# Performance work log

Measured on AMD Instinct MI355X. Metric: run time of the kernel, lower is better.

The kernel has to match this reference:

```python
import jax, jax.numpy as jnp
import numpy as np

B, T, F, H = 256, 128, 32, 1024  # batch, seq_len(=decoder steps), input/output feat, hidden


def lstm_cell(x, h, c, Wih, Whh, b):
    # PyTorch gate order: i, f, g, o
    gates = x @ Wih.T + h @ Whh.T + b  # [B, 4H]
    i, f, g, o = jnp.split(gates, 4, axis=-1)
    i, f, o = jax.nn.sigmoid(i), jax.nn.sigmoid(f), jax.nn.sigmoid(o)
    c_new = f * c + i * jnp.tanh(g)
    h_new = o * jnp.tanh(c_new)
    return h_new, c_new


def setup_inputs() -> dict:
    key = jax.random.key(0)
    ks = jax.random.split(key, 16)
    s = 0.05
    d = {
        "input_seq": jax.random.normal(ks[0], (B, T, F), jnp.float32),
        # encoder LSTM (2 layers); bias = bias_ih + bias_hh folded together
        "enc_Wih0": jax.random.normal(ks[1], (4 * H, F), jnp.float32) * s,
        "enc_Whh0": jax.random.normal(ks[2], (4 * H, H), jnp.float32) * s,
        "enc_b0": jax.random.normal(ks[3], (4 * H,), jnp.float32) * s,
        "enc_Wih1": jax.random.normal(ks[4], (4 * H, H), jnp.float32) * s,
        "enc_Whh1": jax.random.normal(ks[5], (4 * H, H), jnp.float32) * s,
        "enc_b1": jax.random.normal(ks[6], (4 * H,), jnp.float32) * s,
        # decoder LSTM (2 layers), input size = output_size = F
        "dec_Wih0": jax.random.normal(ks[7], (4 * H, F), jnp.float32) * s,
        "dec_Whh0": jax.random.normal(ks[8], (4 * H, H), jnp.float32) * s,
        "dec_b0": jax.random.normal(ks[9], (4 * H,), jnp.float32) * s,
        "dec_Wih1": jax.random.normal(ks[10], (4 * H, H), jnp.float32) * s,
        "dec_Whh1": jax.random.normal(ks[11], (4 * H, H), jnp.float32) * s,
        "dec_b1": jax.random.normal(ks[12], (4 * H,), jnp.float32) * s,
        # output head
        "lin_W": jax.random.normal(ks[13], (F, H), jnp.float32) * s,
        "lin_b": jax.random.normal(ks[14], (F,), jnp.float32) * s,
    }
    return d


def reference(input_seq, enc_Wih0, enc_Whh0, enc_b0, enc_Wih1, enc_Whh1, enc_b1,
              dec_Wih0, dec_Whh0, dec_b0, dec_Wih1, dec_Whh1, dec_b1, lin_W, lin_b):
    Bsz = input_seq.shape[0]
    zeros = jnp.zeros((Bsz, H), input_seq.dtype)

    # ---- encoder: 2-layer LSTM scanned over time ----
    def enc_step(carry, x_t):
        h0, c0, h1, c1 = carry
        h0, c0 = lstm_cell(x_t, h0, c0, enc_Wih0, enc_Whh0, enc_b0)
        h1, c1 = lstm_cell(h0, h1, c1, enc_Wih1, enc_Whh1, enc_b1)
        return (h0, c0, h1, c1), None

    xs = jnp.swapaxes(input_seq, 0, 1)  # [T, B, F]
    (h0, c0, h1, c1), _ = jax.lax.scan(enc_step, (zeros, zeros, zeros, zeros), xs)

    def dec_step(carry, _):
        x, h0, c0, h1, c1 = carry
        h0, c0 = lstm_cell(x, h0, c0, dec_Wih0, dec_Whh0, dec_b0)
        h1, c1 = lstm_cell(h0, h1, c1, dec_Wih1, dec_Whh1, dec_b1)
        out = h1 @ lin_W.T + lin_b  # [B, F]
        return (out, h0, c0, h1, c1), out

    dec_in0 = input_seq[:, -1, :]  # [B, F]
    _, outs = jax.lax.scan(dec_step, (dec_in0, h0, c0, h1, c1), None, length=T)
    return jnp.swapaxes(outs, 0, 1)  # [B, T, F]
```

## Files before the change

kernel.cpp:

```cpp
#include <hip/hip_runtime.h>

typedef _Float16 half_t;
typedef _Float16 half8 __attribute__((ext_vector_type(8)));
typedef _Float16 half4v __attribute__((ext_vector_type(4)));
typedef float f32x4 __attribute__((ext_vector_type(4)));

#define DI __device__ __forceinline__

constexpr int Bsz = 256;
constexpr int Tsz = 128;
constexpr int Fsz = 32;
constexpr int Hsz = 1024;
constexpr int NG  = 4096;
constexpr int K1  = 1152;
constexpr int K2  = 2048;

DI int perm_to_orig(int np) {
    int nt = np >> 6, r = np & 63, g = r >> 4, jo = r & 15;
    return g * Hsz + nt * 16 + jo;
}

DI size_t wfrag(int np, int k) {
    return ((size_t)((k >> 5) * 256 + (np >> 4)) * 64 + ((k >> 3) & 3) * 16 + (np & 15)) * 8 + (k & 7);
}
DI size_t afrag(int b, int k) {
    return ((size_t)((k >> 5) * 16 + (b >> 4)) * 64 + ((k >> 3) & 3) * 16 + (b & 15)) * 8 + (k & 7);
}


__global__ void pack_cat(half_t* __restrict__ dst, const float* __restrict__ srcA, int KA,
                         const float* __restrict__ srcB, int KB, int KP) {
    int tid = threadIdx.x;
    int np = blockIdx.y * 64 + (tid & 63);
    int k0 = (blockIdx.x * 4 + (tid >> 6)) * 8;
    if (k0 >= KP) return;
    int n = perm_to_orig(np);
    half8 v;
#pragma unroll
    for (int j = 0; j < 8; ++j) {
        int k = k0 + j;
        float f = 0.f;
        if (k < KA) f = srcA[(size_t)n * KA + k];
        else if (k < KA + KB) f = srcB[(size_t)n * KB + (k - KA)];
        v[j] = (half_t)f;
    }
    *(half8*)(dst + wfrag(np, k0)) = v;
}

__global__ void pack_fold(half_t* __restrict__ dst, const float* __restrict__ Wih0,
                          const float* __restrict__ linW) {
    __shared__ float lw[32][128];
    __shared__ float wi[16][32];
    int nb = blockIdx.x * 16;
    int jb = blockIdx.y * 128;
    int t = threadIdx.x;
    for (int i = t; i < 32 * 128; i += 256) { int f = i >> 7, j = i & 127; lw[f][j] = linW[f * Hsz + jb + j]; }
    for (int i = t; i < 16 * 32; i += 256) { int r = i >> 5, f = i & 31; wi[r][f] = Wih0[perm_to_orig(nb + r) * 32 + f]; }
    __syncthreads();
    int r = t >> 4, j0 = (t & 15) * 8;
    half8 v;
#pragma unroll
    for (int jj = 0; jj < 8; ++jj) {
        float s = 0.f;
#pragma unroll
        for (int f = 0; f < 32; ++f) s += wi[r][f] * lw[f][j0 + jj];
        v[jj] = (half_t)s;
    }
    *(half8*)(dst + wfrag(nb + r, 1024 + jb + j0)) = v;
}

__global__ void pack_bias(float* __restrict__ b5, const float* eb0, const float* eb1,
                          const float* db0, const float* db1, const float* dWih0,
                          const float* linb) {
    int idx = blockIdx.x * 256 + threadIdx.x;
    if (idx >= 5 * NG) return;
    int which = idx >> 12, np = idx & (NG - 1);
    int n = perm_to_orig(np);
    float v;
    if (which == 0) v = eb0[n];
    else if (which == 1) v = eb1[n];
    else if (which == 2) v = db0[n];
    else if (which == 3) {
        v = db0[n];
        for (int f = 0; f < 32; ++f) v += dWih0[n * 32 + f] * linb[f];
    } else v = db1[n];
    b5[idx] = v;
}

__global__ void pack_small(half_t* __restrict__ Wlin, half_t* __restrict__ bufA0,
                           const float* __restrict__ linW, const float* __restrict__ inseq) {
    int idx = blockIdx.x * 256 + threadIdx.x;
    if (idx < 32 * Hsz) Wlin[idx] = (half_t)linW[idx];
    if (idx < Bsz * 4) {
        int b = idx >> 2, fg = idx & 3;
        half8 v;
#pragma unroll
        for (int j = 0; j < 8; ++j) v[j] = (half_t)inseq[(size_t)b * (Tsz * Fsz) + fg * 8 + j];
        *(half8*)(bufA0 + afrag(b, 1024 + fg * 8)) = v;
    }
}


template <int K>
__launch_bounds__(256, 1) __global__
void lstm_phase(const half_t* __restrict__ A, const half_t* __restrict__ W,
                const float* __restrict__ bias, float* __restrict__ c,
                half_t* __restrict__ hd0, int cb0,
                half_t* __restrict__ hd1, int cb1,
                half_t* __restrict__ hd2, int cb2,
                const float* __restrict__ xsrc, half_t* __restrict__ xdst) {
    constexpr int CHW = (K / 32) / 4;
    __shared__ float red[4][64][68];
    int bid = blockIdx.x;
    int low3 = bid & 7, rest = bid >> 3;
    int mt = rest & 3, nt = ((rest >> 2) << 3) | low3;
    int tid = threadIdx.x, lane = tid & 63, w = tid >> 6;

    const half_t* pa = A + ((size_t)((w * CHW) * 16 + mt * 4) * 64 + lane) * 8;
    const half_t* pw = W + ((size_t)((w * CHW) * 256 + nt * 4) * 64 + lane) * 8;

    f32x4 acc[4][4] = {};
    half8 bA[3][4], bW[3][4];

#define LOADS(st, kk)                                                              \
    {                                                                              \
        _Pragma("unroll") for (int mi = 0; mi < 4; ++mi)                           \
            bA[st][mi] = *(const half8*)(pa + (size_t)(kk) * 8192 + mi * 512);     \
        _Pragma("unroll") for (int ni = 0; ni < 4; ++ni)                           \
            bW[st][ni] = *(const half8*)(pw + (size_t)(kk) * 131072 + ni * 512);   \
    }

    LOADS(0, 0)
    LOADS(1, 1)
#pragma unroll
    for (int kk = 0; kk < CHW; ++kk) {
        if (kk + 2 < CHW) LOADS((kk + 2) % 3, kk + 2)
        const int st = kk % 3;
#pragma unroll
        for (int mi = 0; mi < 4; ++mi)
#pragma unroll
            for (int ni = 0; ni < 4; ++ni)
                acc[mi][ni] = __builtin_amdgcn_mfma_f32_16x16x32_f16(bA[st][mi], bW[st][ni], acc[mi][ni], 0, 0, 0);
    }
#undef LOADS

    int l15 = lane & 15, l4 = lane >> 4;
#pragma unroll
    for (int mi = 0; mi < 4; ++mi)
#pragma unroll
        for (int ni = 0; ni < 4; ++ni)
#pragma unroll
            for (int r = 0; r < 4; ++r)
                red[w][mi * 16 + l4 * 4 + r][ni * 16 + l15] = acc[mi][ni][r];
    __syncthreads();

    int row = tid >> 2, q = tid & 3, jo0 = q * 4;
    f32x4 g0 = {}, g1 = {}, g2 = {}, g3 = {};
#pragma unroll
    for (int ww = 0; ww < 4; ++ww) {
        g0 += *(const f32x4*)&red[ww][row][jo0];
        g1 += *(const f32x4*)&red[ww][row][16 + jo0];
        g2 += *(const f32x4*)&red[ww][row][32 + jo0];
        g3 += *(const f32x4*)&red[ww][row][48 + jo0];
    }
    const float* bb = bias + nt * 64;
    g0 += *(const f32x4*)(bb + jo0);
    g1 += *(const f32x4*)(bb + 16 + jo0);
    g2 += *(const f32x4*)(bb + 32 + jo0);
    g3 += *(const f32x4*)(bb + 48 + jo0);

    int bglob = mt * 64 + row;
    int jg0 = nt * 16 + jo0;
    float* cp = c + (size_t)bglob * Hsz + jg0;
    f32x4 cold = *(const f32x4*)cp;
    f32x4 cnew;
    half4v hv;
#pragma unroll
    for (int e = 0; e < 4; ++e) {
        float si = 1.f / (1.f + __expf(-g0[e]));
        float sf = 1.f / (1.f + __expf(-g1[e]));
        float tg = 1.f - 2.f / (__expf(2.f * g2[e]) + 1.f);
        float so = 1.f / (1.f + __expf(-g3[e]));
        float cn = sf * cold[e] + si * tg;
        cnew[e] = cn;
        float th = 1.f - 2.f / (__expf(2.f * cn) + 1.f);
        hv[e] = (half_t)(so * th);
    }
    *(f32x4*)cp = cnew;

    {
        int col = cb0 + jg0;
        *(half4v*)(hd0 + ((size_t)((col >> 5) * 16 + (bglob >> 4)) * 64 + ((col >> 3) & 3) * 16 + (bglob & 15)) * 8 + (col & 7)) = hv;
    }
    if (hd1) {
        int col = cb1 + jg0;
        *(half4v*)(hd1 + ((size_t)((col >> 5) * 16 + (bglob >> 4)) * 64 + ((col >> 3) & 3) * 16 + (bglob & 15)) * 8 + (col & 7)) = hv;
    }
    if (hd2) {
        int col = cb2 + jg0;
        *(half4v*)(hd2 + ((size_t)((col >> 5) * 16 + (bglob >> 4)) * 64 + ((col >> 3) & 3) * 16 + (bglob & 15)) * 8 + (col & 7)) = hv;
    }

    if (xsrc && nt == 0) {
        int f0 = q * 8;
        const float* xs = xsrc + (size_t)bglob * (Tsz * Fsz) + f0;
        half8 v;
#pragma unroll
        for (int j = 0; j < 8; ++j) v[j] = (half_t)xs[j];
        *(half8*)(xdst + afrag(bglob, 1024 + f0)) = v;
    }
}

__launch_bounds__(256, 1) __global__
void lin_out(const half_t* __restrict__ H1, const half_t* __restrict__ Wl,
             const float* __restrict__ lb, float* __restrict__ out) {
    int w = threadIdx.x >> 6, lane = threadIdx.x & 63;
    int l15 = lane & 15, l4 = lane >> 4;
    int rowt = blockIdx.x * 4 + w;
    int t = rowt >> 4, mi = rowt & 15;
    const half_t* pa = H1 + (size_t)t * (Bsz * Hsz);
    const half_t* pb0 = Wl + (size_t)l15 * Hsz + l4 * 8;
    const half_t* pb1 = Wl + (size_t)(16 + l15) * Hsz + l4 * 8;
    f32x4 ac0 = {}, ac1 = {};
#pragma unroll 4
    for (int kc = 0; kc < 32; ++kc) {
        half8 a = *(const half8*)(pa + ((size_t)(kc * 16 + mi) * 64 + lane) * 8);
        half8 b0 = *(const half8*)(pb0 + kc * 32);
        half8 b1 = *(const half8*)(pb1 + kc * 32);
        ac0 = __builtin_amdgcn_mfma_f32_16x16x32_f16(a, b0, ac0, 0, 0, 0);
        ac1 = __builtin_amdgcn_mfma_f32_16x16x32_f16(a, b1, ac1, 0, 0, 0);
    }
#pragma unroll
    for (int r = 0; r < 4; ++r) {
        int row = rowt * 16 + l4 * 4 + r;
        int b = row & 255;
        size_t o = (size_t)b * (Tsz * Fsz) + t * Fsz;
        out[o + l15] = ac0[r] + lb[l15];
        out[o + 16 + l15] = ac1[r] + lb[16 + l15];
    }
}


extern "C" void kernel_launch(void* const* d_in, const int* in_sizes, int n_in,
                              void* d_out, int out_size, void* d_ws, size_t ws_size,
                              hipStream_t stream) {
    (void)in_sizes; (void)n_in;
    const float* in_seq = (const float*)d_in[0];
    const float* eWih0 = (const float*)d_in[1];
    const float* eWhh0 = (const float*)d_in[2];
    const float* eb0 = (const float*)d_in[3];
    const float* eWih1 = (const float*)d_in[4];
    const float* eWhh1 = (const float*)d_in[5];
    const float* eb1 = (const float*)d_in[6];
    const float* dWih0 = (const float*)d_in[7];
    const float* dWhh0 = (const float*)d_in[8];
    const float* db0 = (const float*)d_in[9];
    const float* dWih1 = (const float*)d_in[10];
    const float* dWhh1 = (const float*)d_in[11];
    const float* db1 = (const float*)d_in[12];
    const float* linW = (const float*)d_in[13];
    const float* linb = (const float*)d_in[14];
    float* out = (float*)d_out;

    char* base = (char*)d_ws;
    size_t off = 0;
    auto alloc = [&](size_t bytes) {
        char* r = base + off;
        off = (off + bytes + 255) & ~(size_t)255;
        return r;
    };
    half_t* Wenc1 = (half_t*)alloc((size_t)NG * K1 * 2);
    half_t* Wenc2 = (half_t*)alloc((size_t)NG * K2 * 2);
    half_t* Wdec1a = (half_t*)alloc((size_t)NG * K1 * 2);
    half_t* Wdec1b = (half_t*)alloc((size_t)NG * K2 * 2);
    half_t* Wdec2 = (half_t*)alloc((size_t)NG * K2 * 2);
    half_t* Wlin = (half_t*)alloc((size_t)32 * Hsz * 2);
    float* bias5 = (float*)alloc((size_t)5 * NG * 4);
    float* c0 = (float*)alloc((size_t)Bsz * Hsz * 4);
    float* c1 = (float*)alloc((size_t)Bsz * Hsz * 4);
    half_t* bufA0 = (half_t*)alloc((size_t)Bsz * K1 * 2);
    half_t* bufA1 = (half_t*)alloc((size_t)Bsz * K1 * 2);
    half_t* bufD0 = (half_t*)alloc((size_t)Bsz * K2 * 2);
    half_t* bufD1 = (half_t*)alloc((size_t)Bsz * K2 * 2);
    half_t* bufB0 = (half_t*)alloc((size_t)Bsz * K2 * 2);
    half_t* bufB1 = (half_t*)alloc((size_t)Bsz * K2 * 2);
    half_t* H1hist = (half_t*)alloc((size_t)Tsz * Bsz * Hsz * 2);

    if (off > ws_size) {
        hipMemsetAsync(d_out, 0, (size_t)out_size * 4, stream);
        return;
    }

    half_t* bufA[2] = {bufA0, bufA1};
    half_t* bufD[2] = {bufD0, bufD1};
    half_t* bufB[2] = {bufB0, bufB1};
    float* be1 = bias5;
    float* be2 = bias5 + NG;
    float* bd1a = bias5 + 2 * NG;
    float* bd1b = bias5 + 3 * NG;
    float* bd2 = bias5 + 4 * NG;

    hipMemsetAsync(c0, 0, (size_t)Bsz * Hsz * 4, stream);
    hipMemsetAsync(c1, 0, (size_t)Bsz * Hsz * 4, stream);
    hipMemsetAsync(bufA0, 0, (size_t)Bsz * K1 * 2, stream);
    hipMemsetAsync(bufA1, 0, (size_t)Bsz * K1 * 2, stream);
    hipMemsetAsync(bufB0, 0, (size_t)Bsz * K2 * 2, stream);

    pack_cat<<<dim3(K1 / 32, NG / 64), 256, 0, stream>>>(Wenc1, eWhh0, 1024, eWih0, 32, K1);
    pack_cat<<<dim3(K2 / 32, NG / 64), 256, 0, stream>>>(Wenc2, eWih1, 1024, eWhh1, 1024, K2);
    pack_cat<<<dim3(K1 / 32, NG / 64), 256, 0, stream>>>(Wdec1a, dWhh0, 1024, dWih0, 32, K1);
    pack_cat<<<dim3(K2 / 32, NG / 64), 256, 0, stream>>>(Wdec1b, dWhh0, 1024, nullptr, 0, K2);
    pack_fold<<<dim3(NG / 16, 1024 / 128), 256, 0, stream>>>(Wdec1b, dWih0, linW);
    pack_cat<<<dim3(K2 / 32, NG / 64), 256, 0, stream>>>(Wdec2, dWih1, 1024, dWhh1, 1024, K2);
    pack_bias<<<(5 * NG + 255) / 256, 256, 0, stream>>>(bias5, eb0, eb1, db0, db1, dWih0, linb);
    pack_small<<<128, 256, 0, stream>>>(Wlin, bufA0, linW, in_seq);

    for (int t = 0; t < Tsz; ++t) {
        int pp = t & 1;
        lstm_phase<K1><<<256, 256, 0, stream>>>(
            bufA[pp], Wenc1, be1, c0,
            bufB[pp], 0, bufA[1 - pp], 0, nullptr, 0,
            nullptr, nullptr);
        int tsel = (t + 1 < Tsz) ? t + 1 : Tsz - 1;
        lstm_phase<K2><<<256, 256, 0, stream>>>(
            bufB[pp], Wenc2, be2, c1,
            bufB[1 - pp], 1024, nullptr, 0, nullptr, 0,
            in_seq + (size_t)tsel * Fsz, bufA[1 - pp]);
    }

    lstm_phase<K1><<<256, 256, 0, stream>>>(
        bufA[0], Wdec1a, bd1a, c0,
        bufB[0], 0, bufD[1], 0, nullptr, 0,
        nullptr, nullptr);
    lstm_phase<K2><<<256, 256, 0, stream>>>(
        bufB[0], Wdec2, bd2, c1,
        bufB[1], 1024, bufD[1], 1024, H1hist, 0,
        nullptr, nullptr);
    for (int t = 1; t < Tsz; ++t) {
        int q = t & 1;
        lstm_phase<K2><<<256, 256, 0, stream>>>(
            bufD[q], Wdec1b, bd1b, c0,
            bufB[q], 0, bufD[1 - q], 0, nullptr, 0,
            nullptr, nullptr);
        lstm_phase<K2><<<256, 256, 0, stream>>>(
            bufB[q], Wdec2, bd2, c1,
            bufB[1 - q], 1024, bufD[1 - q], 1024, H1hist + (size_t)t * Bsz * Hsz, 0,
            nullptr, nullptr);
    }

    lin_out<<<512, 256, 0, stream>>>(H1hist, Wlin, linb, out);
}
```

Baseline: 6.622 ms.

## Fuse all LSTM timestep launches into one persistent cooperative kernel with per-row-tile barriers

Replaces the 512 per-phase kernel launches with a single persistent cooperative kernel that loops over phases. Blocks in the same batch row-tile synchronise through an atomic counter, spinning before they read activations. Weight fragments for the next phase are prefetched before the wait, so weight loads overlap the synchronisation. This removes launch overhead and the full-grid drains between launches, at the cost of spin-wait barriers and a dependence on all 256 blocks being co-resident.

```diff
diff --git a/kernel.cpp b/kernel.cpp
--- a/kernel.cpp
+++ b/kernel.cpp
@@ -14,6 +14,7 @@
 constexpr int NG  = 4096;
 constexpr int K1  = 1152;
 constexpr int K2  = 2048;
+constexpr int RSTR = 84;
 
 DI int perm_to_orig(int np) {
     int nt = np >> 6, r = np & 63, g = r >> 4, jo = r & 15;
@@ -101,40 +102,105 @@
 }
 
 
+struct MegaArgs {
+    const float* in_seq;
+    const half_t *Wenc1, *Wenc2, *Wdec1a, *Wdec1b, *Wdec2;
+    const float *be1, *be2, *bd1a, *bd1b, *bd2;
+    float *c0, *c1;
+    half_t *bufA0, *bufA1, *bufB0, *bufB1, *bufD0, *bufD1, *H1hist;
+    unsigned* cnt;
+};
+
+struct PhaseDesc {
+    const half_t* A; const half_t* W; const float* bias; float* c;
+    half_t* h0; int cb0; half_t* h1; int cb1; half_t* h2; int cb2;
+    const float* xs; half_t* xd; int K;
+};
+
+DI PhaseDesc make_desc(int p, const MegaArgs& g) {
+    PhaseDesc d = {};
+    const half_t* bufA[2] = {g.bufA0, g.bufA1};
+    half_t* bufAm[2] = {g.bufA0, g.bufA1};
+    half_t* bufB[2] = {g.bufB0, g.bufB1};
+    half_t* bufD[2] = {g.bufD0, g.bufD1};
+    if (p < 256) {
+        int t = p >> 1, pp = t & 1;
+        if ((p & 1) == 0) {
+            d.A = bufA[pp]; d.W = g.Wenc1; d.bias = g.be1; d.c = g.c0;
+            d.h0 = bufB[pp]; d.cb0 = 0; d.h1 = bufAm[pp ^ 1]; d.cb1 = 0;
+            d.K = K1;
+        } else {
+            int tsel = (t + 1 < Tsz) ? t + 1 : Tsz - 1;
+            d.A = bufB[pp]; d.W = g.Wenc2; d.bias = g.be2; d.c = g.c1;
+            d.h0 = bufB[pp ^ 1]; d.cb0 = 1024;
+            d.xs = g.in_seq + (size_t)tsel * Fsz; d.xd = bufAm[pp ^ 1];
+            d.K = K2;
+        }
+    } else if (p == 256) {
+        d.A = g.bufA0; d.W = g.Wdec1a; d.bias = g.bd1a; d.c = g.c0;
+        d.h0 = g.bufB0; d.cb0 = 0; d.h1 = g.bufD1; d.cb1 = 0;
+        d.K = K1;
+    } else if (p == 257) {
+        d.A = g.bufB0; d.W = g.Wdec2; d.bias = g.bd2; d.c = g.c1;
+        d.h0 = g.bufB1; d.cb0 = 1024; d.h1 = g.bufD1; d.cb1 = 1024;
+        d.h2 = g.H1hist; d.cb2 = 0;
+        d.K = K2;
+    } else {
+        int t = (p - 256) >> 1, q = t & 1;
+        if ((p & 1) == 0) {
+            d.A = bufD[q]; d.W = g.Wdec1b; d.bias = g.bd1b; d.c = g.c0;
+            d.h0 = bufB[q]; d.cb0 = 0; d.h1 = bufD[q ^ 1]; d.cb1 = 0;
+            d.K = K2;
+        } else {
+            d.A = bufB[q]; d.W = g.Wdec2; d.bias = g.bd2; d.c = g.c1;
+            d.h0 = bufB[q ^ 1]; d.cb0 = 1024; d.h1 = bufD[q ^ 1]; d.cb1 = 1024;
+            d.h2 = g.H1hist + (size_t)t * Bsz * Hsz; d.cb2 = 0;
+            d.K = K2;
+        }
+    }
+    return d;
+}
+
 template <int K>
-__launch_bounds__(256, 1) __global__
-void lstm_phase(const half_t* __restrict__ A, const half_t* __restrict__ W,
-                const float* __restrict__ bias, float* __restrict__ c,
-                half_t* __restrict__ hd0, int cb0,
-                half_t* __restrict__ hd1, int cb1,
-                half_t* __restrict__ hd2, int cb2,
-                const float* __restrict__ xsrc, half_t* __restrict__ xdst) {
+DI void run_phase(const PhaseDesc& d, int mt, int nt, int tid,
+                  unsigned* cnt, unsigned waitTarget,
+                  float (&red)[4][64][RSTR]) {
     constexpr int CHW = (K / 32) / 4;
-    __shared__ float red[4][64][68];
-    int bid = blockIdx.x;
-    int low3 = bid & 7, rest = bid >> 3;
-    int mt = rest & 3, nt = ((rest >> 2) << 3) | low3;
-    int tid = threadIdx.x, lane = tid & 63, w = tid >> 6;
-
-    const half_t* pa = A + ((size_t)((w * CHW) * 16 + mt * 4) * 64 + lane) * 8;
-    const half_t* pw = W + ((size_t)((w * CHW) * 256 + nt * 4) * 64 + lane) * 8;
+    int lane = tid & 63, w = tid >> 6;
+    const half_t* pa = d.A + ((size_t)((w * CHW) * 16 + mt * 4) * 64 + lane) * 8;
+    const half_t* pw = d.W + ((size_t)((w * CHW) * 256 + nt * 4) * 64 + lane) * 8;
 
     f32x4 acc[4][4] = {};
     half8 bA[3][4], bW[3][4];
 
-#define LOADS(st, kk)                                                              \
+#define LOADW(st, kk)                                                              \
+    {                                                                              \
+        _Pragma("unroll") for (int ni = 0; ni < 4; ++ni)                           \
+            bW[st][ni] = *(const half8*)(pw + (size_t)(kk) * 131072 + ni * 512);   \
+    }
+#define LOADA(st, kk)                                                              \
     {                                                                              \
         _Pragma("unroll") for (int mi = 0; mi < 4; ++mi)                           \
             bA[st][mi] = *(const half8*)(pa + (size_t)(kk) * 8192 + mi * 512);     \
-        _Pragma("unroll") for (int ni = 0; ni < 4; ++ni)                           \
-            bW[st][ni] = *(const half8*)(pw + (size_t)(kk) * 131072 + ni * 512);   \
-    }
-
-    LOADS(0, 0)
-    LOADS(1, 1)
+    }
+
+    LOADW(0, 0)
+    LOADW(1, 1)
+
+    if (waitTarget) {
+        if (tid == 0) {
+            while (__hip_atomic_load(cnt, __ATOMIC_RELAXED, __HIP_MEMORY_SCOPE_AGENT) < waitTarget)
+                __builtin_amdgcn_s_sleep(1);
+            __threadfence();
+        }
+        __syncthreads();
+    }
+
+    LOADA(0, 0)
+    LOADA(1, 1)
 #pragma unroll
     for (int kk = 0; kk < CHW; ++kk) {
-        if (kk + 2 < CHW) LOADS((kk + 2) % 3, kk + 2)
+        if (kk + 2 < CHW) { LOADW((kk + 2) % 3, kk + 2) LOADA((kk + 2) % 3, kk + 2) }
         const int st = kk % 3;
 #pragma unroll
         for (int mi = 0; mi < 4; ++mi)
@@ -142,7 +208,8 @@
             for (int ni = 0; ni < 4; ++ni)
                 acc[mi][ni] = __builtin_amdgcn_mfma_f32_16x16x32_f16(bA[st][mi], bW[st][ni], acc[mi][ni], 0, 0, 0);
     }
-#undef LOADS
+#undef LOADW
+#undef LOADA
 
     int l15 = lane & 15, l4 = lane >> 4;
 #pragma unroll
@@ -163,7 +230,7 @@
         g2 += *(const f32x4*)&red[ww][row][32 + jo0];
         g3 += *(const f32x4*)&red[ww][row][48 + jo0];
     }
-    const float* bb = bias + nt * 64;
+    const float* bb = d.bias + nt * 64;
     g0 += *(const f32x4*)(bb + jo0);
     g1 += *(const f32x4*)(bb + 16 + jo0);
     g2 += *(const f32x4*)(bb + 32 + jo0);
@@ -171,7 +238,7 @@
 
     int bglob = mt * 64 + row;
     int jg0 = nt * 16 + jo0;
-    float* cp = c + (size_t)bglob * Hsz + jg0;
+    float* cp = d.c + (size_t)bglob * Hsz + jg0;
     f32x4 cold = *(const f32x4*)cp;
     f32x4 cnew;
     half4v hv;
@@ -189,25 +256,46 @@
     *(f32x4*)cp = cnew;
 
     {
-        int col = cb0 + jg0;
-        *(half4v*)(hd0 + ((size_t)((col >> 5) * 16 + (bglob >> 4)) * 64 + ((col >> 3) & 3) * 16 + (bglob & 15)) * 8 + (col & 7)) = hv;
-    }
-    if (hd1) {
-        int col = cb1 + jg0;
-        *(half4v*)(hd1 + ((size_t)((col >> 5) * 16 + (bglob >> 4)) * 64 + ((col >> 3) & 3) * 16 + (bglob & 15)) * 8 + (col & 7)) = hv;
-    }
-    if (hd2) {
-        int col = cb2 + jg0;
-        *(half4v*)(hd2 + ((size_t)((col >> 5) * 16 + (bglob >> 4)) * 64 + ((col >> 3) & 3) * 16 + (bglob & 15)) * 8 + (col & 7)) = hv;
-    }
-
-    if (xsrc && nt == 0) {
+        int col = d.cb0 + jg0;
+        *(half4v*)(d.h0 + ((size_t)((col >> 5) * 16 + (bglob >> 4)) * 64 + ((col >> 3) & 3) * 16 + (bglob & 15)) * 8 + (col & 7)) = hv;
+    }
+    if (d.h1) {
+        int col = d.cb1 + jg0;
+        *(half4v*)(d.h1 + ((size_t)((col >> 5) * 16 + (bglob >> 4)) * 64 + ((col >> 3) & 3) * 16 + (bglob & 15)) * 8 + (col & 7)) = hv;
+    }
+    if (d.h2) {
+        int col = d.cb2 + jg0;
+        *(half4v*)(d.h2 + ((size_t)((col >> 5) * 16 + (bglob >> 4)) * 64 + ((col >> 3) & 3) * 16 + (bglob & 15)) * 8 + (col & 7)) = hv;
+    }
+
+    if (d.xs && nt == 0) {
         int f0 = q * 8;
-        const float* xs = xsrc + (size_t)bglob * (Tsz * Fsz) + f0;
+        const float* xs = d.xs + (size_t)bglob * (Tsz * Fsz) + f0;
         half8 v;
 #pragma unroll
         for (int j = 0; j < 8; ++j) v[j] = (half_t)xs[j];
-        *(half8*)(xdst + afrag(bglob, 1024 + f0)) = v;
+        *(half8*)(d.xd + afrag(bglob, 1024 + f0)) = v;
+    }
+}
+
+__launch_bounds__(256, 1) __global__ void mega_kernel(MegaArgs g) {
+    __shared__ __align__(16) float red[4][64][RSTR];
+    int bid = blockIdx.x;
+    int low3 = bid & 7, rest = bid >> 3;
+    int mt = rest & 3, nt = ((rest >> 2) << 3) | low3;
+    int tid = threadIdx.x;
+    unsigned* cnt = g.cnt + mt * 64;
+
+#pragma unroll 1
+    for (int p = 0; p < 512; ++p) {
+        PhaseDesc d = make_desc(p, g);
+        if (d.K == K1) run_phase<K1>(d, mt, nt, tid, cnt, (unsigned)(64 * p), red);
+        else           run_phase<K2>(d, mt, nt, tid, cnt, (unsigned)(64 * p), red);
+        __syncthreads();
+        if (tid == 0) {
+            __threadfence();
+            __hip_atomic_fetch_add(cnt, 1u, __ATOMIC_RELEASE, __HIP_MEMORY_SCOPE_AGENT);
+        }
     }
 }
 
@@ -285,15 +373,13 @@
     half_t* bufB0 = (half_t*)alloc((size_t)Bsz * K2 * 2);
     half_t* bufB1 = (half_t*)alloc((size_t)Bsz * K2 * 2);
     half_t* H1hist = (half_t*)alloc((size_t)Tsz * Bsz * Hsz * 2);
+    unsigned* barCnt = (unsigned*)alloc(4 * 64 * sizeof(unsigned));
 
     if (off > ws_size) {
         hipMemsetAsync(d_out, 0, (size_t)out_size * 4, stream);
         return;
     }
 
-    half_t* bufA[2] = {bufA0, bufA1};
-    half_t* bufD[2] = {bufD0, bufD1};
-    half_t* bufB[2] = {bufB0, bufB1};
     float* be1 = bias5;
     float* be2 = bias5 + NG;
     float* bd1a = bias5 + 2 * NG;
@@ -305,6 +391,7 @@
     hipMemsetAsync(bufA0, 0, (size_t)Bsz * K1 * 2, stream);
     hipMemsetAsync(bufA1, 0, (size_t)Bsz * K1 * 2, stream);
     hipMemsetAsync(bufB0, 0, (size_t)Bsz * K2 * 2, stream);
+    hipMemsetAsync(barCnt, 0, 4 * 64 * sizeof(unsigned), stream);
 
     pack_cat<<<dim3(K1 / 32, NG / 64), 256, 0, stream>>>(Wenc1, eWhh0, 1024, eWih0, 32, K1);
     pack_cat<<<dim3(K2 / 32, NG / 64), 256, 0, stream>>>(Wenc2, eWih1, 1024, eWhh1, 1024, K2);
@@ -315,38 +402,19 @@
     pack_bias<<<(5 * NG + 255) / 256, 256, 0, stream>>>(bias5, eb0, eb1, db0, db1, dWih0, linb);
     pack_small<<<128, 256, 0, stream>>>(Wlin, bufA0, linW, in_seq);
 
-    for (int t = 0; t < Tsz; ++t) {
-        int pp = t & 1;
-        lstm_phase<K1><<<256, 256, 0, stream>>>(
-            bufA[pp], Wenc1, be1, c0,
-            bufB[pp], 0, bufA[1 - pp], 0, nullptr, 0,
-            nullptr, nullptr);
-        int tsel = (t + 1 < Tsz) ? t + 1 : Tsz - 1;
-        lstm_phase<K2><<<256, 256, 0, stream>>>(
-            bufB[pp], Wenc2, be2, c1,
-            bufB[1 - pp], 1024, nullptr, 0, nullptr, 0,
-            in_seq + (size_t)tsel * Fsz, bufA[1 - pp]);
-    }
-
-    lstm_phase<K1><<<256, 256, 0, stream>>>(
-        bufA[0], Wdec1a, bd1a, c0,
-        bufB[0], 0, bufD[1], 0, nullptr, 0,
-        nullptr, nullptr);
-    lstm_phase<K2><<<256, 256, 0, stream>>>(
-        bufB[0], Wdec2, bd2, c1,
-        bufB[1], 1024, bufD[1], 1024, H1hist, 0,
-        nullptr, nullptr);
-    for (int t = 1; t < Tsz; ++t) {
-        int q = t & 1;
-        lstm_phase<K2><<<256, 256, 0, stream>>>(
-            bufD[q], Wdec1b, bd1b, c0,
-            bufB[q], 0, bufD[1 - q], 0, nullptr, 0,
-            nullptr, nullptr);
-        lstm_phase<K2><<<256, 256, 0, stream>>>(
-            bufB[q], Wdec2, bd2, c1,
-            bufB[1 - q], 1024, bufD[1 - q], 1024, H1hist + (size_t)t * Bsz * Hsz, 0,
-            nullptr, nullptr);
-    }
+    MegaArgs ma;
+    ma.in_seq = in_seq;
+    ma.Wenc1 = Wenc1; ma.Wenc2 = Wenc2;
+    ma.Wdec1a = Wdec1a; ma.Wdec1b = Wdec1b; ma.Wdec2 = Wdec2;
+    ma.be1 = be1; ma.be2 = be2; ma.bd1a = bd1a; ma.bd1b = bd1b; ma.bd2 = bd2;
+    ma.c0 = c0; ma.c1 = c1;
+    ma.bufA0 = bufA0; ma.bufA1 = bufA1;
+    ma.bufB0 = bufB0; ma.bufB1 = bufB1;
+    ma.bufD0 = bufD0; ma.bufD1 = bufD1;
+    ma.H1hist = H1hist;
+    ma.cnt = barCnt;
+    void* kargs[] = {&ma};
+    hipLaunchCooperativeKernel((const void*)mega_kernel, dim3(256), dim3(256), kargs, 0, stream);
 
     lin_out<<<512, 256, 0, stream>>>(H1hist, Wlin, linb, out);
 }
```

Result: slower. 17.70 ms (+167.3%).
